# Optimization experiments

Measured on AMD Instinct MI355X. Metric: run time of the kernel, lower is better.

## Reference

```python
import jax, jax.numpy as jnp
import numpy as np

B, T, IN = 4096, 512, 1
H, L = 50, 2


def setup_inputs() -> dict:
    key = jax.random.key(0)
    ks = jax.random.split(key, 11)
    s_in = 1.0 / np.sqrt(H)  # PyTorch LSTM init scale
    def u(k, shape):
        return jax.random.uniform(k, shape, jnp.float32, -s_in, s_in)
    return {
        "x": jax.random.normal(ks[0], (B, T, IN), jnp.float32),
        # layer 0 (gate order i, f, g, o stacked along first axis, like torch)
        "W_ih0": u(ks[1], (4 * H, IN)),
        "W_hh0": u(ks[2], (4 * H, H)),
        "b_ih0": u(ks[3], (4 * H,)),
        "b_hh0": u(ks[4], (4 * H,)),
        # layer 1
        "W_ih1": u(ks[5], (4 * H, H)),
        "W_hh1": u(ks[6], (4 * H, H)),
        "b_ih1": u(ks[7], (4 * H,)),
        "b_hh1": u(ks[8], (4 * H,)),
        # final linear projection hidden -> 1
        "fc_w": u(ks[9], (1, H)),
        "fc_b": u(ks[10], (1,)),
    }


def _lstm_layer(x_tbf, W_ih, W_hh, b_ih, b_hh):
    """x_tbf: [T, B, F] -> outputs [T, B, H]. Zero initial (h, c)."""
    # Precompute input contribution for all timesteps at once: [T, B, 4H]
    gates_x = jnp.einsum('tbf,gf->tbg', x_tbf, W_ih) + b_ih + b_hh

    def step(carry, gx):
        h, c = carry
        g = gx + h @ W_hh.T  # [B, 4H]
        i, f, gg, o = jnp.split(g, 4, axis=-1)
        i = jax.nn.sigmoid(i)
        f = jax.nn.sigmoid(f)
        gg = jnp.tanh(gg)
        o = jax.nn.sigmoid(o)
        c = f * c + i * gg
        h = o * jnp.tanh(c)
        return (h, c), h

    Bsz = x_tbf.shape[1]
    h0 = jnp.zeros((Bsz, W_hh.shape[1]), x_tbf.dtype)
    (_, _), hs = jax.lax.scan(step, (h0, h0), gates_x)
    return hs  # [T, B, H]


def reference(x, W_ih0, W_hh0, b_ih0, b_hh0, W_ih1, W_hh1, b_ih1, b_hh1, fc_w, fc_b):
    x_tbf = jnp.transpose(x, (1, 0, 2))  # [T, B, IN]
    h1 = _lstm_layer(x_tbf, W_ih0, W_hh0, b_ih0, b_hh0)   # [T, B, H]
    h2 = _lstm_layer(h1, W_ih1, W_hh1, b_ih1, b_hh1)      # [T, B, H]
    last = h2[-1]                                         # [B, H] == out[:, -1, :]
    return last @ fc_w.T + fc_b                           # [B, 1]
```

## Files before the change

### kernel.cpp

```cpp
#include <hip/hip_runtime.h>


typedef _Float16 half8 __attribute__((ext_vector_type(8)));
typedef float    f32x4 __attribute__((ext_vector_type(4)));

#define TT   512
#define HID  50
#define NB   16
#define LOG2E 1.44269504f

__device__ __forceinline__ float4 make_wfrag(const float* W, const float* Wx,
                                             int gate, int cell, int chunk,
                                             int quad, bool foldx, float scale) {
    half8 hv = {};
    #pragma unroll
    for (int j = 0; j < 8; ++j) {
        const int k = 32 * chunk + 8 * quad + j;
        float v = 0.0f;
        if (cell < HID) {
            if (k < HID)                 v = W[(gate * HID + cell) * HID + k] * scale;
            else if (foldx && k == HID)  v = Wx[gate * HID + cell] * scale;
        }
        hv[j] = (_Float16)v;
    }
    return __builtin_bit_cast(float4, hv);
}

__device__ __forceinline__ float cell_update(const f32x4 a, float& c) {
    const float ei = __builtin_amdgcn_exp2f(a[0]);
    const float ef = __builtin_amdgcn_exp2f(a[1]);
    const float eg = __builtin_amdgcn_exp2f(a[2]);
    const float eo = __builtin_amdgcn_exp2f(a[3]);
    const float itg = (eg - 1.0f) *
        __builtin_amdgcn_rcpf((1.0f + ei) * (eg + 1.0f));
    const float sf = __builtin_amdgcn_rcpf(1.0f + ef);
    c = sf * c + itg;
    const float ec = __builtin_amdgcn_exp2f(c * (2.0f * LOG2E));
    return (ec - 1.0f) *
        __builtin_amdgcn_rcpf((1.0f + eo) * (ec + 1.0f));
}

#define PIN(f) asm volatile("" : "+v"(f.x), "+v"(f.y), "+v"(f.z), "+v"(f.w));
#define MFMA(af, b, c) __builtin_amdgcn_mfma_f32_16x16x32_f16(__builtin_bit_cast(half8, (af)), (b), (c), 0, 0, 0)

extern "C" __global__ __launch_bounds__(832, 4)
void lstm2_mfma_kernel(const float* __restrict__ x,
                       const float* __restrict__ W_ih0, const float* __restrict__ W_hh0,
                       const float* __restrict__ b_ih0, const float* __restrict__ b_hh0,
                       const float* __restrict__ W_ih1, const float* __restrict__ W_hh1,
                       const float* __restrict__ b_ih1, const float* __restrict__ b_hh1,
                       const float* __restrict__ fc_w, const float* __restrict__ fc_b,
                       float* __restrict__ out)
{
    __shared__ _Float16 H0[2][1024];
    __shared__ _Float16 H1[2][1024];
    __shared__ float    hfin[HID * NB];

    const int tid  = threadIdx.x;
    const int lane = tid & 63;
    const int wv   = tid >> 6;
    const int b0   = blockIdx.x * NB;

    for (int i = tid; i < 1024; i += 832) {
        H0[0][i] = (_Float16)0.f; H0[1][i] = (_Float16)0.f;
        H1[0][i] = (_Float16)0.f; H1[1][i] = (_Float16)0.f;
    }

    const int quad = lane >> 4;
    const int col  = lane & 15;

    const int mrow  = lane & 15;
    const int gateA = mrow & 3;
    const int cellA = 4 * wv + (mrow >> 2);
    const float scA = (gateA == 2) ? 2.0f * LOG2E : -LOG2E;
    float4 A0c0 = make_wfrag(W_hh0, W_ih0, gateA, cellA, 0, quad, true,  scA);
    float4 A0c1 = make_wfrag(W_hh0, W_ih0, gateA, cellA, 1, quad, true,  scA);
    float4 Aic0 = make_wfrag(W_ih1, W_ih1, gateA, cellA, 0, quad, false, scA);
    float4 Aic1 = make_wfrag(W_ih1, W_ih1, gateA, cellA, 1, quad, false, scA);
    float4 Ahc0 = make_wfrag(W_hh1, W_hh1, gateA, cellA, 0, quad, false, scA);
    float4 Ahc1 = make_wfrag(W_hh1, W_hh1, gateA, cellA, 1, quad, false, scA);
    PIN(A0c0) PIN(A0c1) PIN(Aic0) PIN(Aic1) PIN(Ahc0) PIN(Ahc1)

    const int  cellD = 4 * wv + quad;
    const bool ewok  = (cellD < HID);
    f32x4 bias0, bias1;
    #pragma unroll
    for (int g = 0; g < 4; ++g) {
        const float s = (g == 2) ? 2.0f * LOG2E : -LOG2E;
        bias0[g] = ewok ? (b_ih0[g * HID + cellD] + b_hh0[g * HID + cellD]) * s : 0.f;
        bias1[g] = ewok ? (b_ih1[g * HID + cellD] + b_hh1[g * HID + cellD]) * s : 0.f;
    }
    const int wi = (cellD >> 5) * 512 + (((cellD & 31) >> 3) * 16 + col) * 8 + (cellD & 7);

    if (tid < NB) H0[0][512 + (32 + tid) * 8 + 2] = (_Float16)x[(size_t)(b0 + tid) * TT];

    float c0 = 0.f, c1 = 0.f;
    __syncthreads();

    #pragma unroll 2
    for (int u = 0; u <= TT; ++u) {
        const int pu = u & 1, pn = pu ^ 1;

        half8 b0c0 = *(half8*)(&H0[pu][lane * 8]);
        half8 b0c1 = *(half8*)(&H0[pu][512 + lane * 8]);

        float xr = 0.f;
        if (tid < NB && (u + 1) < TT)
            xr = x[(size_t)(b0 + tid) * TT + u + 1];

        if (u != TT) {
            f32x4 acc = bias0;
            acc = MFMA(A0c0, b0c0, acc);
            acc = MFMA(A0c1, b0c1, acc);
            const float h = cell_update(acc, c0);
            if (ewok) H0[pn][wi] = (_Float16)h;
        }
        if (u != 0) {
            half8 b1c0 = *(half8*)(&H1[pn][lane * 8]);
            half8 b1c1 = *(half8*)(&H1[pn][512 + lane * 8]);
            f32x4 acc = bias1;
            acc = MFMA(Aic0, b0c0, acc);
            acc = MFMA(Aic1, b0c1, acc);
            acc = MFMA(Ahc0, b1c0, acc);
            acc = MFMA(Ahc1, b1c1, acc);
            const float h = cell_update(acc, c1);
            if (ewok) {
                H1[pu][wi] = (_Float16)h;
                if (u == TT) hfin[cellD * NB + col] = h;
            }
        }
        if (tid < NB && (u + 1) < TT)
            H0[pn][512 + (32 + tid) * 8 + 2] = (_Float16)xr;
        __syncthreads();
    }

    if (tid < NB) {
        float s = fc_b[0];
        for (int k = 0; k < HID; ++k)
            s += fc_w[k] * hfin[k * NB + tid];
        out[b0 + tid] = s;
    }
}

extern "C" void kernel_launch(void* const* d_in, const int* in_sizes, int n_in,
                              void* d_out, int out_size, void* d_ws, size_t ws_size,
                              hipStream_t stream) {
    (void)in_sizes; (void)n_in; (void)d_ws; (void)ws_size; (void)out_size;
    const float* x     = (const float*)d_in[0];
    const float* W_ih0 = (const float*)d_in[1];
    const float* W_hh0 = (const float*)d_in[2];
    const float* b_ih0 = (const float*)d_in[3];
    const float* b_hh0 = (const float*)d_in[4];
    const float* W_ih1 = (const float*)d_in[5];
    const float* W_hh1 = (const float*)d_in[6];
    const float* b_ih1 = (const float*)d_in[7];
    const float* b_hh1 = (const float*)d_in[8];
    const float* fc_w  = (const float*)d_in[9];
    const float* fc_b  = (const float*)d_in[10];

    dim3 grid(4096 / NB);
    dim3 block(832);
    lstm2_mfma_kernel<<<grid, block, 0, stream>>>(
        x, W_ih0, W_hh0, b_ih0, b_hh0,
        W_ih1, W_hh1, b_ih1, b_hh1,
        fc_w, fc_b, (float*)d_out);
}
```

Baseline: 414.5 us.

## Halve batch per block and pack both layers' cell updates into one lane set

Batch per block drops from 16 to 8, so the 16 MFMA columns are split: lanes 0-7 hold layer-0 results and lanes 8-15 take layer-1 results, moved over with a DPP row swap. Each lane then runs a single shared transcendental cell update instead of two, which shortens the serial per-step critical path. Launch bounds are raised to target more resident blocks. The cost is twice as many blocks with half of each MFMA's columns unused, plus redundant MFMA work on invalid first and last steps.

```diff
diff --git a/kernel.cpp b/kernel.cpp
--- a/kernel.cpp
+++ b/kernel.cpp
@@ -6,7 +6,7 @@
 
 #define TT   512
 #define HID  50
-#define NB   16
+#define NB   8
 #define LOG2E 1.44269504f
 
 __device__ __forceinline__ float4 make_wfrag(const float* W, const float* Wx,
@@ -26,24 +26,16 @@
     return __builtin_bit_cast(float4, hv);
 }
 
-__device__ __forceinline__ float cell_update(const f32x4 a, float& c) {
-    const float ei = __builtin_amdgcn_exp2f(a[0]);
-    const float ef = __builtin_amdgcn_exp2f(a[1]);
-    const float eg = __builtin_amdgcn_exp2f(a[2]);
-    const float eo = __builtin_amdgcn_exp2f(a[3]);
-    const float itg = (eg - 1.0f) *
-        __builtin_amdgcn_rcpf((1.0f + ei) * (eg + 1.0f));
-    const float sf = __builtin_amdgcn_rcpf(1.0f + ef);
-    c = sf * c + itg;
-    const float ec = __builtin_amdgcn_exp2f(c * (2.0f * LOG2E));
-    return (ec - 1.0f) *
-        __builtin_amdgcn_rcpf((1.0f + eo) * (ec + 1.0f));
+__device__ __forceinline__ float xor8(float v) {
+    int i = __builtin_bit_cast(int, v);
+    i = __builtin_amdgcn_mov_dpp(i, 0x128, 0xF, 0xF, true);
+    return __builtin_bit_cast(float, i);
 }
 
 #define PIN(f) asm volatile("" : "+v"(f.x), "+v"(f.y), "+v"(f.z), "+v"(f.w));
 #define MFMA(af, b, c) __builtin_amdgcn_mfma_f32_16x16x32_f16(__builtin_bit_cast(half8, (af)), (b), (c), 0, 0, 0)
 
-extern "C" __global__ __launch_bounds__(832, 4)
+extern "C" __global__ __launch_bounds__(832, 6)
 void lstm2_mfma_kernel(const float* __restrict__ x,
                        const float* __restrict__ W_ih0, const float* __restrict__ W_hh0,
                        const float* __restrict__ b_ih0, const float* __restrict__ b_hh0,
@@ -68,6 +60,8 @@
 
     const int quad = lane >> 4;
     const int col  = lane & 15;
+    const int col8 = col & 7;
+    const bool isL0 = (col < 8);
 
     const int mrow  = lane & 15;
     const int gateA = mrow & 3;
@@ -90,11 +84,11 @@
         bias0[g] = ewok ? (b_ih0[g * HID + cellD] + b_hh0[g * HID + cellD]) * s : 0.f;
         bias1[g] = ewok ? (b_ih1[g * HID + cellD] + b_hh1[g * HID + cellD]) * s : 0.f;
     }
-    const int wi = (cellD >> 5) * 512 + (((cellD & 31) >> 3) * 16 + col) * 8 + (cellD & 7);
+    const int wi = (cellD >> 5) * 512 + (((cellD & 31) >> 3) * 16 + col8) * 8 + (cellD & 7);
 
     if (tid < NB) H0[0][512 + (32 + tid) * 8 + 2] = (_Float16)x[(size_t)(b0 + tid) * TT];
 
-    float c0 = 0.f, c1 = 0.f;
+    float cst = 0.f;
     __syncthreads();
 
     #pragma unroll 2
@@ -103,32 +97,47 @@
 
         half8 b0c0 = *(half8*)(&H0[pu][lane * 8]);
         half8 b0c1 = *(half8*)(&H0[pu][512 + lane * 8]);
+        half8 b1c0 = *(half8*)(&H1[pn][lane * 8]);
+        half8 b1c1 = *(half8*)(&H1[pn][512 + lane * 8]);
 
         float xr = 0.f;
         if (tid < NB && (u + 1) < TT)
             xr = x[(size_t)(b0 + tid) * TT + u + 1];
 
-        if (u != TT) {
-            f32x4 acc = bias0;
-            acc = MFMA(A0c0, b0c0, acc);
-            acc = MFMA(A0c1, b0c1, acc);
-            const float h = cell_update(acc, c0);
-            if (ewok) H0[pn][wi] = (_Float16)h;
+        f32x4 acc0 = bias0;
+        acc0 = MFMA(A0c0, b0c0, acc0);
+        acc0 = MFMA(A0c1, b0c1, acc0);
+        f32x4 acc1 = bias1;
+        acc1 = MFMA(Aic0, b0c0, acc1);
+        acc1 = MFMA(Aic1, b0c1, acc1);
+        acc1 = MFMA(Ahc0, b1c0, acc1);
+        acc1 = MFMA(Ahc1, b1c1, acc1);
+
+        f32x4 am;
+        #pragma unroll
+        for (int r = 0; r < 4; ++r) {
+            const float sw = xor8(acc1[r]);
+            am[r] = isL0 ? acc0[r] : sw;
         }
-        if (u != 0) {
-            half8 b1c0 = *(half8*)(&H1[pn][lane * 8]);
-            half8 b1c1 = *(half8*)(&H1[pn][512 + lane * 8]);
-            f32x4 acc = bias1;
-            acc = MFMA(Aic0, b0c0, acc);
-            acc = MFMA(Aic1, b0c1, acc);
-            acc = MFMA(Ahc0, b1c0, acc);
-            acc = MFMA(Ahc1, b1c1, acc);
-            const float h = cell_update(acc, c1);
-            if (ewok) {
-                H1[pu][wi] = (_Float16)h;
-                if (u == TT) hfin[cellD * NB + col] = h;
-            }
-        }
+        const bool valid = isL0 ? (u != TT) : (u != 0);
+
+        const float ei = __builtin_amdgcn_exp2f(am[0]);
+        const float ef = __builtin_amdgcn_exp2f(am[1]);
+        const float eg = __builtin_amdgcn_exp2f(am[2]);
+        const float eo = __builtin_amdgcn_exp2f(am[3]);
+        const float itg = (eg - 1.0f) *
+            __builtin_amdgcn_rcpf((1.0f + ei) * (eg + 1.0f));
+        const float sf = __builtin_amdgcn_rcpf(1.0f + ef);
+        const float cn = sf * cst + itg;
+        const float ec = __builtin_amdgcn_exp2f(cn * (2.0f * LOG2E));
+        const float h  = (ec - 1.0f) *
+            __builtin_amdgcn_rcpf((1.0f + eo) * (ec + 1.0f));
+
+        if (valid) cst = cn;
+        _Float16* dst = isL0 ? &H0[pn][wi] : &H1[pu][wi];
+        if (valid && ewok) *dst = (_Float16)h;
+        if (u == TT && !isL0 && ewok) hfin[cellD * NB + col8] = h;
+
         if (tid < NB && (u + 1) < TT)
             H0[pn][512 + (32 + tid) * 8 + 2] = (_Float16)xr;
         __syncthreads();
```

After: 606.8 us. 46.4% more time.
